# Optimization experiments

Measured on AMD Instinct MI355X. Metric: run time of the kernel, lower is better.

## Reference

```python
import jax, jax.numpy as jnp
import numpy as np

N_OPS, B, C, N = 7, 128, 64, 30   # n_ops from alphas (7), SPD dim hard-coded to 30 in source
KARCHER_ITERS = 3                 # fixed-point iterations of the weighted geometric mean


def _spd_fn(X, fn):
    """Apply scalar fn to eigenvalues of batched symmetric matrices X[..., n, n]."""
    s, U = jnp.linalg.eigh(X)
    s = jnp.maximum(s, 1e-8)  # SPD clamp for log/sqrt stability
    return jnp.einsum('...ij,...j,...kj->...ik', U, fn(s), U)


def _sym(X):
    return 0.5 * (X + jnp.swapaxes(X, -1, -2))


def setup_inputs() -> dict:
    key = jax.random.key(0)
    k1, k2 = jax.random.split(key)
    # Candidate-op outputs: SPD matrices, one per (op, batch, channel).
    G = jax.random.normal(k1, (N_OPS, B, C, N, N), dtype=jnp.float32)
    spds = jnp.einsum('...ij,...kj->...ik', G, G) / N + 0.1 * jnp.eye(N, dtype=jnp.float32)
    # Architecture logits for this edge (softmaxed in forward, as in Network.forward).
    alphas = 0.001 * jax.random.normal(k2, (N_OPS,), dtype=jnp.float32)
    return {"spds": spds, "alphas": alphas}


def reference(spds, alphas):
    """MixedOp forward: softmax-weighted SPD geometric (Karcher) barycenter over
    candidate ops, batched over every (batch, channel) 30x30 SPD matrix.
    Replaces the per-channel Python loop + bary_geom_weightedbatch of the source.
    Returns [B, C, N, N]."""
    w = jax.nn.softmax(alphas)                       # [n_ops]
    A = spds.reshape(N_OPS, B * C, N, N)             # [o, m, n, n], m = B*C
    # init with weighted arithmetic mean (standard Karcher-flow initialization)
    X = jnp.einsum('o,omij->mij', w, A)              # [m, n, n]
    for _ in range(KARCHER_ITERS):
        Xh = _spd_fn(X, jnp.sqrt)                    # X^{1/2}
        Xih = _spd_fn(X, lambda s: 1.0 / jnp.sqrt(s))  # X^{-1/2}
        mid = jnp.einsum('mij,omjk,mkl->omil', Xih, A, Xih)  # [o, m, n, n]
        logs = _spd_fn(_sym(mid), jnp.log)
        L = _sym(jnp.einsum('o,omij->mij', w, logs))  # tangent-space mean
        X = _sym(Xh @ _spd_fn(L, jnp.exp) @ Xh)      # exp map back to manifold
    return X.reshape(B, C, N, N)
```

## Files before the change

### kernel.cpp

```cpp
#include <hip/hip_runtime.h>
#include <math.h>

#define NOPS 7
#define KITERS 3
#define NBLK 31
#define WPB 4
#define CHKFROM 6
#define CONVEPS 1e-5f

#define WFENCE() asm volatile("" ::: "memory")
#define VSYNC() asm volatile("s_waitcnt vmcnt(0)" ::: "memory")

template<int M> __device__ __forceinline__ float xshuf(float x);
template<> __device__ __forceinline__ float xshuf<1>(float x) {
    return __int_as_float(__builtin_amdgcn_mov_dpp(__float_as_int(x), 0xB1, 0xF, 0xF, true));
}
template<> __device__ __forceinline__ float xshuf<2>(float x) {
    return __int_as_float(__builtin_amdgcn_mov_dpp(__float_as_int(x), 0x4E, 0xF, 0xF, true));
}
template<> __device__ __forceinline__ float xshuf<4>(float x) {
    return __int_as_float(__builtin_amdgcn_ds_swizzle(__float_as_int(x), (4 << 10) | 0x1F));
}
template<> __device__ __forceinline__ float xshuf<8>(float x) {
    return __int_as_float(__builtin_amdgcn_ds_swizzle(__float_as_int(x), (8 << 10) | 0x1F));
}

template<int M>
__device__ __forceinline__ void jround(float (&a)[16], float (&v)[16], float2* ct,
                                       const int il, const int wlane, const int fKb) {
    const int fil = (il & (M - 1)) | ((il >> 1) & ~(M - 1));
    const float dq  = xshuf<M>(a[0]);
    const float apq = a[M];
    float th = (dq - a[0]) * __builtin_amdgcn_rcpf(apq + apq);
    float t  = copysignf(__builtin_amdgcn_rcpf(
                   fabsf(th) + __builtin_amdgcn_sqrtf(fmaf(th, th, 1.f))), th);
    float cc = __builtin_amdgcn_rsqf(fmaf(t, t, 1.f));
    float ss = t * cc;
    if (!(fabsf(apq) > 1e-12f)) { cc = 1.f; ss = 0.f; }
    if ((wlane & (32 | M)) == 0) ct[fil] = make_float2(cc, ss);
    WFENCE();
    const float2 me = ct[fil];
    const float sg = (il & M) ? 1.f : -1.f;
    const float c0 = me.x, s0 = sg * me.y;
    const int fb = fil ^ fKb;
    const float4* cup = (const float4*)(ct + fKb);
    float4 q;
    #pragma unroll
    for (int j = 0; j < 16; ++j) {
        if (j & M) continue;
        const int fj = (j & (M - 1)) | ((j >> 1) & ~(M - 1));
        const float2 cs = ct[fb ^ fj];
        const float sl = sg * cs.y;
        const float ak = a[j], am = a[j ^ M];
        a[j]     = fmaf( sl, am, cs.x * ak);
        a[j ^ M] = fmaf(-sl, ak, cs.x * am);
        if ((fj & 1) == 0) q = cup[fj >> 1];
        const float cux = (fj & 1) ? q.z : q.x;
        const float cuy = (fj & 1) ? q.w : q.y;
        const float vk = v[j], vm = v[j ^ M];
        v[j]     = fmaf(-cuy, vm, cux * vk);
        v[j ^ M] = fmaf( cuy, vk, cux * vm);
    }
    #pragma unroll
    for (int j = 0; j < 16; ++j) {
        if (j & M) continue;
        const float r1 = xshuf<M>(a[j ^ M]);
        const float r2 = xshuf<M>(a[j]);
        a[j]     = fmaf(s0, r1, c0 * a[j]);
        a[j ^ M] = fmaf(s0, r2, c0 * a[j ^ M]);
    }
}

__global__ __launch_bounds__(64 * WPB)
void karcher_kernel(const float* __restrict__ spds, const float* __restrict__ alphas,
                    float* __restrict__ out, int Mtot) {
    __shared__ __align__(16) float XIb[WPB][1024];
    __shared__ __align__(16) float SCb[WPB][1024];
    __shared__ __align__(64) float2 CTb[WPB][16];
    __shared__ float FDAb[WPB][32];
    __shared__ float FDBb[WPB][32];
    __shared__ float WSb[WPB][8];

    const int tid   = threadIdx.x;
    const int wid   = tid >> 6;
    const int wlane = tid & 63;
    const int il    = wlane & 31;
    const int cbit  = wlane >> 5;
    const int cbase = cbit << 4;
    const int fKb   = cbit << 3;
    const int c13   = cbit ? 13 : 0;
    const int mat   = blockIdx.x * WPB + wid;
    const bool rr   = (il < 30);

    float* XI  = XIb[wid];
    float* SC  = SCb[wid];
    float2* CT = CTb[wid];
    float* FDA = FDAb[wid];
    float* FDB = FDBb[wid];
    float* WS  = WSb[wid];

    if (mat >= Mtot) return;

    if (wlane == 0) {
        float aa[NOPS], mx = -1e30f, sum = 0.f;
        #pragma unroll
        for (int o = 0; o < NOPS; ++o) { aa[o] = alphas[o]; mx = fmaxf(mx, aa[o]); }
        #pragma unroll
        for (int o = 0; o < NOPS; ++o) { aa[o] = expf(aa[o] - mx); sum += aa[o]; }
        #pragma unroll
        for (int o = 0; o < NOPS; ++o) WS[o] = aa[o] / sum;
    }

    int l4row = il;
    #pragma unroll
    for (int i = 0; i < 4; ++i) l4row = ((l4row << 1) & 31) ^ ((l4row & 16) ? 5 : 0);

    const size_t ostr = (size_t)Mtot * 900;
    const float* Abase = spds + (size_t)mat * 900 + (size_t)il * 30 + cbase;
    float* orow = out + (size_t)mat * 900 + (size_t)il * 30 + cbase;

    auto stage16 = [&](float* buf, const float (&r)[16]) {
        #pragma unroll
        for (int j = 0; j < 16; ++j) buf[((cbase + j) << 5) + il] = r[j];
    };
    auto xload16 = [&](const float* buf, float (&a)[16]) {
        #pragma unroll
        for (int j = 0; j < 16; ++j) a[j] = buf[((il ^ (cbase + j)) << 5) + il];
    };
    auto perm4 = [&](float (&a)[16], float (&v)[16]) {
        constexpr int L4T[16] = {0,16,5,21,10,26,15,31,20,4,17,1,30,14,27,11};
        #pragma unroll
        for (int j = 0; j < 16; ++j) SC[((cbase + j) << 5) + il] = a[j];
        WFENCE();
        #pragma unroll
        for (int j = 0; j < 16; ++j) a[j] = SC[((L4T[j] ^ c13) << 5) + l4row];
        WFENCE();
        #pragma unroll
        for (int j = 0; j < 16; ++j) SC[((cbase + j) << 5) + il] = v[j];
        WFENCE();
        #pragma unroll
        for (int j = 0; j < 16; ++j) v[j] = SC[((L4T[j] ^ c13) << 5) + il];
        WFENCE();
    };
    auto jacobi = [&](float (&a)[16], float (&v)[16]) {
        #pragma unroll
        for (int j = 0; j < 16; ++j) v[j] = (cbase + j == il) ? 1.f : 0.f;
        #pragma unroll 1
        for (int b = 0; b < NBLK; ++b) {
            jround<1>(a, v, CT, il, wlane, fKb);
            jround<2>(a, v, CT, il, wlane, fKb);
            jround<4>(a, v, CT, il, wlane, fKb);
            jround<8>(a, v, CT, il, wlane, fKb);
            if (b >= CHKFROM) {
                float mx = cbit ? fabsf(a[0]) : 0.f;
                #pragma unroll
                for (int j = 1; j < 16; ++j) mx = fmaxf(mx, fabsf(a[j]));
                if (!__any(mx > CONVEPS)) break;
            }
            if (b != NBLK - 1) perm4(a, v);
        }
    };
    auto loadA = [&](const float* Ao, float (&r)[16]) {
        #pragma unroll
        for (int u = 0; u < 7; ++u) {
            const float2 p = *(const float2*)(Ao + 2 * u);
            r[2 * u] = p.x; r[2 * u + 1] = p.y;
        }
        if (cbit == 0) {
            const float2 p = *(const float2*)(Ao + 14);
            r[14] = p.x; r[15] = p.y;
        }
    };
    auto fma16 = [&](const float* buf, const int k, const float c, float (&acc)[16]) {
        const float4* bp = (const float4*)(buf + (k << 5) + cbase);
        #pragma unroll
        for (int q = 0; q < 4; ++q) {
            const float4 b = bp[q];
            acc[4*q+0] = fmaf(c, b.x, acc[4*q+0]);
            acc[4*q+1] = fmaf(c, b.y, acc[4*q+1]);
            acc[4*q+2] = fmaf(c, b.z, acc[4*q+2]);
            acc[4*q+3] = fmaf(c, b.w, acc[4*q+3]);
        }
    };

    WFENCE();

    float X[16];
    #pragma unroll
    for (int j = 0; j < 16; ++j) X[j] = 0.f;
    if (rr) {
        #pragma unroll 1
        for (int o = 0; o < NOPS; ++o) {
            const float wo = WS[o];
            float r[16];
            #pragma unroll
            for (int j = 0; j < 16; ++j) r[j] = 0.f;
            loadA(Abase + (size_t)o * ostr, r);
            #pragma unroll
            for (int j = 0; j < 16; ++j) X[j] = fmaf(wo, r[j], X[j]);
        }
    }

    float Lacc[16];

    #pragma unroll 1
    for (int it = 0; it < KITERS; ++it) {
        WFENCE();
        stage16(SC, X);
        WFENCE();
        float a1[16], v1[16];
        xload16(SC, a1);
        jacobi(a1, v1);
        if (wlane < 32) {
            const float lam = fmaxf(a1[0], 1e-8f);
            const float sq = sqrtf(lam);
            FDA[il] = sq;
            FDB[il] = 1.f / sq;
        }
        WFENCE();
        stage16(SC, v1);
        WFENCE();
        {
            float xh[16], xi[16];
            #pragma unroll
            for (int j = 0; j < 16; ++j) { xh[j] = 0.f; xi[j] = 0.f; }
            #pragma unroll 2
            for (int k = 0; k < 32; ++k) {
                const float vk = SC[(k << 5) + il];
                const float c1 = FDA[k] * vk;
                const float c2 = FDB[k] * vk;
                const float4* bp = (const float4*)(SC + (k << 5) + cbase);
                #pragma unroll
                for (int q = 0; q < 4; ++q) {
                    const float4 b = bp[q];
                    xh[4*q+0] = fmaf(c1, b.x, xh[4*q+0]); xi[4*q+0] = fmaf(c2, b.x, xi[4*q+0]);
                    xh[4*q+1] = fmaf(c1, b.y, xh[4*q+1]); xi[4*q+1] = fmaf(c2, b.y, xi[4*q+1]);
                    xh[4*q+2] = fmaf(c1, b.z, xh[4*q+2]); xi[4*q+2] = fmaf(c2, b.z, xi[4*q+2]);
                    xh[4*q+3] = fmaf(c1, b.w, xh[4*q+3]); xi[4*q+3] = fmaf(c2, b.w, xi[4*q+3]);
                }
            }
            if (rr) {
                #pragma unroll
                for (int u = 0; u < 7; ++u)
                    *(float2*)(orow + 2 * u) = make_float2(xh[2*u], xh[2*u+1]);
                if (cbit == 0)
                    *(float2*)(orow + 14) = make_float2(xh[14], xh[15]);
            }
            WFENCE();
            stage16(XI, xi);
        }
        #pragma unroll
        for (int j = 0; j < 16; ++j) Lacc[j] = 0.f;

        #pragma unroll 1
        for (int o = 0; o < NOPS; ++o) {
            float ar[16];
            #pragma unroll
            for (int j = 0; j < 16; ++j) ar[j] = 0.f;
            if (rr) loadA(Abase + (size_t)o * ostr, ar);
            WFENCE();
            stage16(SC, ar);
            WFENCE();
            float T[16];
            #pragma unroll
            for (int j = 0; j < 16; ++j) T[j] = 0.f;
            #pragma unroll 2
            for (int k = 0; k < 30; ++k)
                fma16(SC, k, XI[(k << 5) + il], T);
            WFENCE();
            stage16(SC, T);
            WFENCE();
            float md[16];
            #pragma unroll
            for (int j = 0; j < 16; ++j) md[j] = 0.f;
            #pragma unroll 2
            for (int k = 0; k < 30; ++k)
                fma16(XI, k, SC[(k << 5) + il], md);
            WFENCE();
            stage16(SC, md);
            WFENCE();
            float a2[16], v2[16];
            xload16(SC, a2);
            jacobi(a2, v2);
            if (wlane < 32) FDA[il] = logf(fmaxf(a2[0], 1e-8f));
            WFENCE();
            stage16(SC, v2);
            WFENCE();
            const float wo = WS[o];
            #pragma unroll 2
            for (int k = 0; k < 32; ++k)
                fma16(SC, k, wo * FDA[k] * SC[(k << 5) + il], Lacc);
        }

        WFENCE();
        stage16(SC, Lacc);
        WFENCE();
        float a3[16], v3[16];
        xload16(SC, a3);
        jacobi(a3, v3);
        if (wlane < 32) FDA[il] = expf(fmaxf(a3[0], 1e-8f));
        WFENCE();
        stage16(SC, v3);
        WFENCE();
        float E[16];
        #pragma unroll
        for (int j = 0; j < 16; ++j) E[j] = 0.f;
        #pragma unroll 2
        for (int k = 0; k < 32; ++k)
            fma16(SC, k, FDA[k] * SC[(k << 5) + il], E);
        float xr[16];
        #pragma unroll
        for (int j = 0; j < 16; ++j) xr[j] = 0.f;
        VSYNC();
        if (rr) loadA(orow, xr);
        WFENCE();
        stage16(XI, E);
        stage16(SC, xr);
        WFENCE();
        float T2[16];
        #pragma unroll
        for (int j = 0; j < 16; ++j) T2[j] = 0.f;
        #pragma unroll 2
        for (int k = 0; k < 30; ++k)
            fma16(XI, k, SC[(k << 5) + il], T2);
        WFENCE();
        stage16(XI, T2);
        WFENCE();
        #pragma unroll
        for (int j = 0; j < 16; ++j) X[j] = 0.f;
        #pragma unroll 2
        for (int k = 0; k < 30; ++k)
            fma16(SC, k, XI[(k << 5) + il], X);
    }

    if (rr) {
        #pragma unroll
        for (int u = 0; u < 7; ++u)
            *(float2*)(orow + 2 * u) = make_float2(X[2*u], X[2*u+1]);
        if (cbit == 0)
            *(float2*)(orow + 14) = make_float2(X[14], X[15]);
    }
}

extern "C" void kernel_launch(void* const* d_in, const int* in_sizes, int n_in,
                              void* d_out, int out_size, void* d_ws, size_t ws_size,
                              hipStream_t stream) {
    const float* spds   = (const float*)d_in[0];
    const float* alphas = (const float*)d_in[1];
    float* out = (float*)d_out;
    const int Mtot = in_sizes[0] / (NOPS * 900);
    karcher_kernel<<<dim3((Mtot + WPB - 1) / WPB), dim3(64 * WPB), 0, stream>>>(
        spds, alphas, out, Mtot);
}
```

Before: 7.846 ms.

## Vectorize Jacobi rotation coefficient loads and check convergence earlier with looser tolerance

```diff
diff --git a/kernel.cpp b/kernel.cpp
--- a/kernel.cpp
+++ b/kernel.cpp
@@ -5,8 +5,8 @@
 #define KITERS 3
 #define NBLK 31
 #define WPB 4
-#define CHKFROM 6
-#define CONVEPS 1e-5f
+#define CHKFROM 4
+#define CONVEPS 3e-5f
 
 #define WFENCE() asm volatile("" ::: "memory")
 #define VSYNC() asm volatile("s_waitcnt vmcnt(0)" ::: "memory")
@@ -42,24 +42,41 @@
     const float2 me = ct[fil];
     const float sg = (il & M) ? 1.f : -1.f;
     const float c0 = me.x, s0 = sg * me.y;
-    const int fb = fil ^ fKb;
+    const int  fb = fil ^ fKb;
+    const bool fo = (fb & 1);
+    const int  fbE = fb & ~1;
     const float4* cup = (const float4*)(ct + fKb);
-    float4 q;
     #pragma unroll
-    for (int j = 0; j < 16; ++j) {
-        if (j & M) continue;
-        const int fj = (j & (M - 1)) | ((j >> 1) & ~(M - 1));
-        const float2 cs = ct[fb ^ fj];
-        const float sl = sg * cs.y;
-        const float ak = a[j], am = a[j ^ M];
-        a[j]     = fmaf( sl, am, cs.x * ak);
-        a[j ^ M] = fmaf(-sl, ak, cs.x * am);
-        if ((fj & 1) == 0) q = cup[fj >> 1];
-        const float cux = (fj & 1) ? q.z : q.x;
-        const float cuy = (fj & 1) ? q.w : q.y;
-        const float vk = v[j], vm = v[j ^ M];
-        v[j]     = fmaf(-cuy, vm, cux * vk);
-        v[j ^ M] = fmaf( cuy, vk, cux * vm);
+    for (int P = 0; P < 4; ++P) {
+        const int fjA = 2 * P, fjB = 2 * P + 1;
+        const int jA = (fjA & (M - 1)) | ((fjA & ~(M - 1)) << 1);
+        const int jB = (fjB & (M - 1)) | ((fjB & ~(M - 1)) << 1);
+        const float4 g = *(const float4*)(ct + (fbE ^ fjA));
+        const float csAx = fo ? g.z : g.x, csAy = fo ? g.w : g.y;
+        const float csBx = fo ? g.x : g.z, csBy = fo ? g.y : g.w;
+        {
+            const float sl = sg * csAy;
+            const float ak = a[jA], am = a[jA ^ M];
+            a[jA]     = fmaf( sl, am, csAx * ak);
+            a[jA ^ M] = fmaf(-sl, ak, csAx * am);
+        }
+        {
+            const float sl = sg * csBy;
+            const float ak = a[jB], am = a[jB ^ M];
+            a[jB]     = fmaf( sl, am, csBx * ak);
+            a[jB ^ M] = fmaf(-sl, ak, csBx * am);
+        }
+        const float4 q = cup[P];
+        {
+            const float vk = v[jA], vm = v[jA ^ M];
+            v[jA]     = fmaf(-q.y, vm, q.x * vk);
+            v[jA ^ M] = fmaf( q.y, vk, q.x * vm);
+        }
+        {
+            const float vk = v[jB], vm = v[jB ^ M];
+            v[jB]     = fmaf(-q.w, vm, q.z * vk);
+            v[jB ^ M] = fmaf( q.w, vk, q.z * vm);
+        }
     }
     #pragma unroll
     for (int j = 0; j < 16; ++j) {
```

Result: slower. 8.069 ms (+2.8%).
